# Kernel optimization log

Hardware: AMD Instinct MI355X
Metric: run time of the kernel (lower is better)

## Reference

```python
import jax, jax.numpy as jnp
import numpy as np

N_USERS = 50000
N_ITEMS = 75000
N_NODES = N_USERS + N_ITEMS
NNZ = 1250000
EMB = 64
N_LAYERS = 3
BATCH = 4096
EPS = 1e-12


def setup_inputs() -> dict:
    key = jax.random.key(0)
    ks = jax.random.split(key, 12)
    xavier = float(np.sqrt(6.0 / (EMB + EMB)))
    return {
        "user": jax.random.randint(ks[0], (BATCH,), 0, N_USERS, dtype=jnp.int64 if jax.config.jax_enable_x64 else jnp.int32),
        "pos_item": jax.random.randint(ks[1], (BATCH,), 0, N_ITEMS, dtype=jnp.int32),
        "neg_item": jax.random.randint(ks[2], (BATCH,), 0, N_ITEMS, dtype=jnp.int32),
        "row": jax.random.randint(ks[3], (NNZ,), 0, N_NODES, dtype=jnp.int32),
        "col": jax.random.randint(ks[4], (NNZ,), 0, N_NODES, dtype=jnp.int32),
        "vals": jax.random.uniform(ks[5], (NNZ,), dtype=jnp.float32),
        "emb": jax.random.normal(ks[6], (N_NODES, EMB), dtype=jnp.float32) * 0.1,
        "W1": jax.random.uniform(ks[7], (N_LAYERS, EMB, EMB), minval=-xavier, maxval=xavier, dtype=jnp.float32),
        "b1": jnp.zeros((N_LAYERS, EMB), dtype=jnp.float32),
        "W2": jax.random.uniform(ks[8], (N_LAYERS, EMB, EMB), minval=-xavier, maxval=xavier, dtype=jnp.float32),
        "b2": jnp.zeros((N_LAYERS, EMB), dtype=jnp.float32),
    }


def _l2_normalize(x):
    n = jnp.linalg.norm(x, axis=-1, keepdims=True)
    return x / jnp.maximum(n, EPS)


def reference(user, pos_item, neg_item, row, col, vals, emb, W1, b1, W2, b2):
    # eval mode: node_dropout / mess_dropout inactive (rates 0)
    node_feat = emb
    all_embeddings = [node_feat]
    for l in range(N_LAYERS):
        # sparse SpMM: agg[i] = sum_j A[i,j] * node_feat[j]
        msg = vals[:, None] * node_feat[col]            # [nnz, d]
        agg = jax.ops.segment_sum(msg, row, num_segments=N_NODES)  # [N, d]
        part_1 = jax.nn.leaky_relu(agg @ W1[l].T + b1[l], 0.2)
        part_2 = jax.nn.leaky_relu((agg * node_feat) @ W2[l].T + b2[l], 0.2)
        node_feat = part_1 + part_2
        all_embeddings.append(_l2_normalize(node_feat))
    embedding_weight = jnp.concatenate(all_embeddings, axis=-1)  # [N, 4*d]
    gcn_user = embedding_weight[:N_USERS]
    gcn_item = embedding_weight[N_USERS:]
    return (gcn_user[user], gcn_item[pos_item], gcn_item[neg_item])
```

## Files before the change

kernel.cpp:

```cpp
#include <hip/hip_runtime.h>
#include <hip/hip_fp16.h>

#define N_USERS 50000
#define N_ITEMS 75000
#define N_NODES 125000
#define N_PAD   125008
#define NNZ     1250000
#define EMB     64
#define N_LAYERS 3
#define BATCH   4096
#define CONCAT  256

#define BROWS   128
#define NB      ((N_NODES + BROWS - 1) / BROWS)
#define CHUNK   4096
#define NCHUNK  ((NNZ + CHUNK - 1) / CHUNK)
#define EPT     (CHUNK / 256)
#define BCAP    1600
#define FB_NODES 32
#define SCAP    8

#define F4      (N_NODES * EMB / 4)
#define G4      (3 * BATCH * EMB / 4)
#define SM      (3 * BATCH)
#define INIT_ITEMS (F4 + G4 + SM)
#define INIT_BLOCKS ((INIT_ITEMS + 255) / 256)

typedef _Float16 half8  __attribute__((ext_vector_type(8)));
typedef _Float16 half4  __attribute__((ext_vector_type(4)));
typedef float    floatx4 __attribute__((ext_vector_type(4)));

__device__ __forceinline__ bool user_is_i64(const void* uptr) {
    const int* u = (const int*)uptr;
    return (u[1] | u[3] | u[5] | u[7]) == 0;
}
__device__ __forceinline__ int load_user(const void* uptr, int b, bool is64) {
    return is64 ? (int)((const long long*)uptr)[b] : ((const int*)uptr)[b];
}
__device__ __forceinline__ int sample_node(const void* user, const int* pos,
                                           const int* neg, int which, int b,
                                           bool is64) {
    if (which == 0) return load_user(user, b, is64);
    return N_USERS + (which == 1 ? pos[b] : neg[b]);
}

__device__ __forceinline__ float unpack_val(unsigned w) {
    unsigned short us = (unsigned short)(w >> 17);
    _Float16 h = __builtin_bit_cast(_Float16, us);
    return (float)h;
}

__global__ __launch_bounds__(256) void part_init_kernel(
    const int* __restrict__ row, const int* __restrict__ col,
    const float* __restrict__ vals, const float* __restrict__ emb,
    const void* __restrict__ user, const int* __restrict__ pos,
    const int* __restrict__ neg,
    _Float16* __restrict__ f16, float* __restrict__ out,
    int* __restrict__ bcnt, int* __restrict__ scnt, int* __restrict__ smap,
    unsigned long long* __restrict__ sw8) {

    __shared__ int h[NB];
    __shared__ int base[NB];

    if (blockIdx.x < NCHUNK) {
        int t = threadIdx.x;
        int e0 = blockIdx.x * CHUNK;
        int e1 = e0 + CHUNK; if (e1 > NNZ) e1 = NNZ;
        for (int i = t; i < NB; i += 256) h[i] = 0;
        __syncthreads();

        unsigned long long rec[EPT];
        int bkt[EPT];
        int ps[EPT];
        int cnt = 0;
        for (int e = e0 + t; e < e1; e += 256) {
            int r = row[e];
            int b = r >> 7;
            _Float16 hv = (_Float16)vals[e];
            unsigned hb = (unsigned)__builtin_bit_cast(unsigned short, hv);
            rec[cnt] = ((unsigned long long)hb << 24)
                     | ((unsigned)(r & 127) << 17)
                     | (unsigned)col[e];
            bkt[cnt] = b;
            ps[cnt] = atomicAdd(&h[b], 1);
            ++cnt;
        }
        __syncthreads();
        for (int i = t; i < NB; i += 256) {
            int c = h[i];
            if (c) base[i] = atomicAdd(&bcnt[i], c);
        }
        __syncthreads();
        for (int k = 0; k < cnt; ++k) {
            int b = bkt[k];
            sw8[(size_t)b * BCAP + base[b] + ps[k]] = rec[k];
        }
    } else {
        int idx = (blockIdx.x - NCHUNK) * 256 + threadIdx.x;
        bool is64 = user_is_i64(user);
        if (idx < F4) {
            floatx4 v = *(const floatx4*)(emb + (size_t)idx * 4);
            half4 o;
            #pragma unroll
            for (int i = 0; i < 4; ++i) o[i] = (_Float16)v[i];
            *(half4*)(f16 + (size_t)idx * 4) = o;
        } else if (idx < F4 + G4) {
            int j = idx - F4;
            int which = j / (BATCH * 16);
            int rem   = j % (BATCH * 16);
            int bb = rem >> 4, c4 = rem & 15;
            int node = sample_node(user, pos, neg, which, bb, is64);
            floatx4 v = *(const floatx4*)(emb + (size_t)node * EMB + c4 * 4);
            *(floatx4*)(out + (size_t)(which * BATCH + bb) * CONCAT + c4 * 4) = v;
        } else if (idx < F4 + G4 + SM) {
            int g2 = idx - F4 - G4;
            int which = g2 / BATCH, bb = g2 % BATCH;
            int node = sample_node(user, pos, neg, which, bb, is64);
            int slot = atomicAdd(&scnt[node], 1);
            if (slot < SCAP) smap[node * SCAP + slot] = g2;
        }
    }
}

__global__ __launch_bounds__(256) void bucket_sort_kernel(
    const int* __restrict__ bcnt,
    const unsigned long long* __restrict__ sw8,
    unsigned* __restrict__ se, int* __restrict__ off, int* __restrict__ endv) {
    __shared__ unsigned long long ew[BCAP];
    __shared__ unsigned eo[BCAP];
    __shared__ int rh[BROWS], rb[BROWS], rc[BROWS];
    __shared__ int s[256];

    int b = blockIdx.x, t = threadIdx.x;
    int n = bcnt[b];
    int s0 = b * BCAP;
    if (t < BROWS) rh[t] = 0;
    __syncthreads();
    const unsigned long long* src = sw8 + (size_t)b * BCAP;
    for (int i = t; i < n; i += 256) {
        unsigned long long rec = src[i];
        ew[i] = rec;
        atomicAdd(&rh[(int)((rec >> 17) & 127)], 1);
    }
    __syncthreads();
    s[t] = (t < BROWS) ? rh[t] : 0;
    __syncthreads();
    for (int d = 1; d < 256; d <<= 1) {
        int x = (t >= d) ? s[t - d] : 0;
        __syncthreads();
        s[t] += x;
        __syncthreads();
    }
    if (t < BROWS) {
        int excl = s[t] - rh[t];
        rb[t] = excl;
        rc[t] = 0;
        int r = b * BROWS + t;
        if (r < N_NODES) {
            off[r]  = s0 + excl;
            endv[r] = s0 + s[t];
        }
    }
    __syncthreads();
    for (int i = t; i < n; i += 256) {
        unsigned long long rec = ew[i];
        int r = (int)((rec >> 17) & 127);
        int p = rb[r] + atomicAdd(&rc[r], 1);
        eo[p] = (unsigned)(((rec >> 24) << 17) | (rec & 0x1FFFFULL));
    }
    __syncthreads();
    for (int i = t; i < n; i += 256)
        se[(size_t)s0 + i] = eo[i];
}

__global__ __launch_bounds__(256) void layer_kernel(
    const int* __restrict__ off, const int* __restrict__ endv,
    const unsigned* __restrict__ se,
    const _Float16* __restrict__ fin, _Float16* __restrict__ fout,
    const float* __restrict__ W1, const float* __restrict__ b1,
    const float* __restrict__ W2, const float* __restrict__ b2,
    const int* __restrict__ scnt, const int* __restrict__ smap,
    float* __restrict__ out, int layer) {

    __shared__ _Float16 wlds[2][EMB][EMB];
    __shared__ _Float16 alds[FB_NODES][EMB];

    int tid = threadIdx.x;

    {
        const float* Wsrc0 = W1 + layer * EMB * EMB;
        const float* Wsrc1 = W2 + layer * EMB * EMB;
        #pragma unroll
        for (int m = 0; m < 2; ++m) {
            const float* Ws = m ? Wsrc1 : Wsrc0;
            for (int c = tid; c < 512; c += 256) {
                int n = c >> 3, c16 = c & 7;
                const float* p = Ws + n * EMB + c16 * 8;
                floatx4 wa = *(const floatx4*)p, wb = *(const floatx4*)(p + 4);
                half8 h;
                #pragma unroll
                for (int i = 0; i < 4; ++i) {
                    h[i] = (_Float16)wa[i]; h[4 + i] = (_Float16)wb[i];
                }
                *(half8*)(&wlds[m][n][(c16 ^ (n & 7)) * 8]) = h;
            }
        }
    }

    int wave = tid >> 6, lane = tid & 63;
    int g = lane >> 3;
    int k = lane & 7;
    int base = blockIdx.x * FB_NODES;
    int ln = wave * 8 + g;
    int node = base + ln;
    bool valid = node < N_NODES;

    int j   = valid ? off[node]  : 0;
    int end = valid ? endv[node] : 0;

    float acc[8] = {0.f, 0.f, 0.f, 0.f, 0.f, 0.f, 0.f, 0.f};
    const _Float16* fink = fin + k * 8;

    while (__any(j < end)) {
        unsigned ev[8];
        #pragma unroll
        for (int t = 0; t < 8; ++t)
            ev[t] = (j + t < end) ? se[j + t] : 0u;
        half8 h[8];
        #pragma unroll
        for (int t = 0; t < 8; ++t) {
            int c = (int)(ev[t] & 0x1FFFFu);
            h[t] = *(const half8*)(fink + (size_t)c * EMB);
        }
        #pragma unroll
        for (int t = 0; t < 8; ++t) {
            float val = unpack_val(ev[t]);
            #pragma unroll
            for (int i = 0; i < 8; ++i)
                acc[i] += (float)h[t][i] * val;
        }
        j += 8;
    }

    {
        half8 o;
        #pragma unroll
        for (int i = 0; i < 8; ++i) o[i] = (_Float16)acc[i];
        *(half8*)(&alds[ln][(k ^ (ln & 7)) * 8]) = o;
    }
    __syncthreads();

    if (wave < 2) {
        int lm = lane & 15, quad = lane >> 4;
        int ln0 = wave * 16 + lm;
        int nb = base + wave * 16;
        int nodeD = nb + lm;
        int sw = lm & 7;

        half8 a0 = *(const half8*)(&alds[ln0][(quad ^ sw) * 8]);
        half8 a1 = *(const half8*)(&alds[ln0][((quad + 4) ^ sw) * 8]);

        int nsafe = nodeD < N_NODES ? nodeD : 0;
        const half8* fp = (const half8*)(fin + (size_t)nsafe * EMB + quad * 8);
        half8 f0 = fp[0], f1 = fp[4];
        half8 g0 = a0 * f0, g1 = a1 * f1;

        float nfv[4][4];
        float sq[4] = {0.f, 0.f, 0.f, 0.f};

        #pragma unroll
        for (int t = 0; t < 4; ++t) {
            int n = t * 16 + lm;
            float bias1 = b1[layer * EMB + n];
            float bias2 = b2[layer * EMB + n];
            half8 w10 = *(const half8*)(&wlds[0][n][(quad ^ sw) * 8]);
            half8 w11 = *(const half8*)(&wlds[0][n][((quad + 4) ^ sw) * 8]);
            half8 w20 = *(const half8*)(&wlds[1][n][(quad ^ sw) * 8]);
            half8 w21 = *(const half8*)(&wlds[1][n][((quad + 4) ^ sw) * 8]);
            floatx4 d1 = {0.f, 0.f, 0.f, 0.f}, d2 = {0.f, 0.f, 0.f, 0.f};
            d1 = __builtin_amdgcn_mfma_f32_16x16x32_f16(a0, w10, d1, 0, 0, 0);
            d1 = __builtin_amdgcn_mfma_f32_16x16x32_f16(a1, w11, d1, 0, 0, 0);
            d2 = __builtin_amdgcn_mfma_f32_16x16x32_f16(g0, w20, d2, 0, 0, 0);
            d2 = __builtin_amdgcn_mfma_f32_16x16x32_f16(g1, w21, d2, 0, 0, 0);
            int dim = t * 16 + lm;
            #pragma unroll
            for (int r = 0; r < 4; ++r) {
                int nodeO = nb + quad * 4 + r;
                float p1v = d1[r] + bias1;
                p1v = p1v > 0.f ? p1v : 0.2f * p1v;
                float p2v = d2[r] + bias2;
                p2v = p2v > 0.f ? p2v : 0.2f * p2v;
                float nf = p1v + p2v;
                nfv[t][r] = nf;
                sq[r] += nf * nf;
                if (layer != N_LAYERS - 1 && nodeO < N_NODES)
                    fout[(size_t)nodeO * EMB + dim] = (_Float16)nf;
            }
        }

        #pragma unroll
        for (int r = 0; r < 4; ++r) {
            float v = sq[r];
            #pragma unroll
            for (int m = 1; m < 16; m <<= 1) v += __shfl_xor(v, m, 64);
            sq[r] = fmaxf(sqrtf(v), 1e-12f);
        }

        #pragma unroll
        for (int r = 0; r < 4; ++r) {
            int nodeO = nb + quad * 4 + r;
            if (nodeO >= N_NODES) continue;
            int c = scnt[nodeO]; c = c < SCAP ? c : SCAP;
            float inv = 1.0f / sq[r];
            for (int i2 = 0; i2 < c; ++i2) {
                int smp = smap[nodeO * SCAP + i2];
                float* po = out + (size_t)smp * CONCAT + (layer + 1) * EMB;
                #pragma unroll
                for (int t = 0; t < 4; ++t)
                    po[t * 16 + lm] = nfv[t][r] * inv;
            }
        }
    }
}

extern "C" void kernel_launch(void* const* d_in, const int* in_sizes, int n_in,
                              void* d_out, int out_size, void* d_ws, size_t ws_size,
                              hipStream_t stream) {
    const void* user = d_in[0];
    const int* pos  = (const int*)d_in[1];
    const int* neg  = (const int*)d_in[2];
    const int* row  = (const int*)d_in[3];
    const int* col  = (const int*)d_in[4];
    const float* vals = (const float*)d_in[5];
    const float* emb  = (const float*)d_in[6];
    const float* W1   = (const float*)d_in[7];
    const float* b1   = (const float*)d_in[8];
    const float* W2   = (const float*)d_in[9];
    const float* b2   = (const float*)d_in[10];

    _Float16* f16a   = (_Float16*)d_ws;
    _Float16* f16b   = f16a + (size_t)N_PAD * EMB;
    int*      off    = (int*)(f16b + (size_t)N_PAD * EMB);
    int*      endv   = off + (N_NODES + 8);
    int*      bcnt   = endv + (N_NODES + 8);
    int*      scnt   = bcnt + 984;
    int*      smap   = scnt + N_NODES;
    unsigned long long* sw8 = (unsigned long long*)(smap + N_NODES * SCAP);
    unsigned* se     = (unsigned*)(sw8 + (size_t)NB * BCAP);

    float* out = (float*)d_out;

    hipMemsetAsync(bcnt, 0, (size_t)(984 + N_NODES) * sizeof(int), stream);

    part_init_kernel<<<NCHUNK + INIT_BLOCKS, 256, 0, stream>>>(
        row, col, vals, emb, user, pos, neg, f16a, out, bcnt, scnt, smap, sw8);

    bucket_sort_kernel<<<NB, 256, 0, stream>>>(bcnt, sw8, se, off, endv);

    const _Float16* fin = f16a;
    _Float16* fout = f16b;
    for (int l = 0; l < N_LAYERS; ++l) {
        layer_kernel<<<(N_NODES + FB_NODES - 1) / FB_NODES, 256, 0, stream>>>(
            off, endv, se, fin, fout, W1, b1, W2, b2, scnt, smap, out, l);
        const _Float16* tmp = fout; fout = (_Float16*)fin; fin = (const _Float16*)tmp;
    }
}
```

Baseline: 245.9 us.

## Reorder nodes by degree class and process 64 nodes per block

After: 268.0 us. 1.09x slower.

```diff
diff --git a/kernel.cpp b/kernel.cpp
--- a/kernel.cpp
+++ b/kernel.cpp
@@ -17,8 +17,10 @@
 #define NCHUNK  ((NNZ + CHUNK - 1) / CHUNK)
 #define EPT     (CHUNK / 256)
 #define BCAP    1600
-#define FB_NODES 32
+#define FB_NODES 64
+#define NT64    ((N_NODES + FB_NODES - 1) / FB_NODES)
 #define SCAP    8
+#define NCLS    8
 
 #define F4      (N_NODES * EMB / 4)
 #define G4      (3 * BATCH * EMB / 4)
@@ -125,16 +127,19 @@
 __global__ __launch_bounds__(256) void bucket_sort_kernel(
     const int* __restrict__ bcnt,
     const unsigned long long* __restrict__ sw8,
-    unsigned* __restrict__ se, int* __restrict__ off, int* __restrict__ endv) {
+    unsigned* __restrict__ se, int* __restrict__ off, int* __restrict__ endv,
+    int* __restrict__ classcnt) {
     __shared__ unsigned long long ew[BCAP];
     __shared__ unsigned eo[BCAP];
     __shared__ int rh[BROWS], rb[BROWS], rc[BROWS];
     __shared__ int s[256];
+    __shared__ int ch[NCLS];
 
     int b = blockIdx.x, t = threadIdx.x;
     int n = bcnt[b];
     int s0 = b * BCAP;
     if (t < BROWS) rh[t] = 0;
+    if (t >= BROWS && t < BROWS + NCLS) ch[t - BROWS] = 0;
     __syncthreads();
     const unsigned long long* src = sw8 + (size_t)b * BCAP;
     for (int i = t; i < n; i += 256) {
@@ -159,9 +164,12 @@
         if (r < N_NODES) {
             off[r]  = s0 + excl;
             endv[r] = s0 + s[t];
-        }
-    }
-    __syncthreads();
+            int c = (rh[t] + 7) >> 3; if (c > NCLS - 1) c = NCLS - 1;
+            atomicAdd(&ch[c], 1);
+        }
+    }
+    __syncthreads();
+    if (t < NCLS && ch[t]) atomicAdd(&classcnt[t], ch[t]);
     for (int i = t; i < n; i += 256) {
         unsigned long long rec = ew[i];
         int r = (int)((rec >> 17) & 127);
@@ -173,9 +181,35 @@
         se[(size_t)s0 + i] = eo[i];
 }
 
+__global__ __launch_bounds__(256) void perm_kernel(
+    const int* __restrict__ off, const int* __restrict__ endv,
+    const int* __restrict__ classcnt, int* __restrict__ classpos,
+    int* __restrict__ perm) {
+    __shared__ int lh[NCLS], lbase[NCLS];
+    int t = threadIdx.x;
+    int node = blockIdx.x * 256 + t;
+    if (t < NCLS) lh[t] = 0;
+    __syncthreads();
+    int c = -1, lpos = 0;
+    if (node < N_NODES) {
+        int deg = endv[node] - off[node];
+        c = (deg + 7) >> 3; if (c > NCLS - 1) c = NCLS - 1;
+        lpos = atomicAdd(&lh[c], 1);
+    }
+    __syncthreads();
+    if (t < NCLS) {
+        int sbase = 0;
+        #pragma unroll
+        for (int i = 0; i < NCLS; ++i) if (i < t) sbase += classcnt[i];
+        lbase[t] = sbase + (lh[t] ? atomicAdd(&classpos[t], lh[t]) : 0);
+    }
+    __syncthreads();
+    if (node < N_NODES) perm[lbase[c] + lpos] = node;
+}
+
 __global__ __launch_bounds__(256) void layer_kernel(
     const int* __restrict__ off, const int* __restrict__ endv,
-    const unsigned* __restrict__ se,
+    const unsigned* __restrict__ se, const int* __restrict__ perm,
     const _Float16* __restrict__ fin, _Float16* __restrict__ fout,
     const float* __restrict__ W1, const float* __restrict__ b1,
     const float* __restrict__ W2, const float* __restrict__ b2,
@@ -211,38 +245,36 @@
     int g = lane >> 3;
     int k = lane & 7;
     int base = blockIdx.x * FB_NODES;
-    int ln = wave * 8 + g;
-    int node = base + ln;
-    bool valid = node < N_NODES;
-
-    int j   = valid ? off[node]  : 0;
-    int end = valid ? endv[node] : 0;
-
-    float acc[8] = {0.f, 0.f, 0.f, 0.f, 0.f, 0.f, 0.f, 0.f};
     const _Float16* fink = fin + k * 8;
 
-    while (__any(j < end)) {
-        unsigned ev[8];
-        #pragma unroll
-        for (int t = 0; t < 8; ++t)
-            ev[t] = (j + t < end) ? se[j + t] : 0u;
-        half8 h[8];
-        #pragma unroll
-        for (int t = 0; t < 8; ++t) {
-            int c = (int)(ev[t] & 0x1FFFFu);
-            h[t] = *(const half8*)(fink + (size_t)c * EMB);
-        }
-        #pragma unroll
-        for (int t = 0; t < 8; ++t) {
-            float val = unpack_val(ev[t]);
-            #pragma unroll
-            for (int i = 0; i < 8; ++i)
-                acc[i] += (float)h[t][i] * val;
-        }
-        j += 8;
-    }
-
-    {
+    for (int p = 0; p < 2; ++p) {
+        int ln = p * 32 + wave * 8 + g;
+        int idx = base + ln;
+        int node = (idx < N_NODES) ? perm[idx] : -1;
+        int j = 0, end = 0;
+        if (node >= 0) { j = off[node]; end = endv[node]; }
+
+        float acc[8] = {0.f, 0.f, 0.f, 0.f, 0.f, 0.f, 0.f, 0.f};
+        while (__any(j < end)) {
+            unsigned ev[8];
+            #pragma unroll
+            for (int t = 0; t < 8; ++t)
+                ev[t] = (j + t < end) ? se[j + t] : 0u;
+            half8 h[8];
+            #pragma unroll
+            for (int t = 0; t < 8; ++t) {
+                int c = (int)(ev[t] & 0x1FFFFu);
+                h[t] = *(const half8*)(fink + (size_t)c * EMB);
+            }
+            #pragma unroll
+            for (int t = 0; t < 8; ++t) {
+                float val = unpack_val(ev[t]);
+                #pragma unroll
+                for (int i = 0; i < 8; ++i)
+                    acc[i] += (float)h[t][i] * val;
+            }
+            j += 8;
+        }
         half8 o;
         #pragma unroll
         for (int i = 0; i < 8; ++i) o[i] = (_Float16)acc[i];
@@ -250,17 +282,17 @@
     }
     __syncthreads();
 
-    if (wave < 2) {
+    {
         int lm = lane & 15, quad = lane >> 4;
         int ln0 = wave * 16 + lm;
-        int nb = base + wave * 16;
-        int nodeD = nb + lm;
+        int idxD = base + ln0;
+        int nodeD = (idxD < N_NODES) ? perm[idxD] : -1;
         int sw = lm & 7;
 
         half8 a0 = *(const half8*)(&alds[ln0][(quad ^ sw) * 8]);
         half8 a1 = *(const half8*)(&alds[ln0][((quad + 4) ^ sw) * 8]);
 
-        int nsafe = nodeD < N_NODES ? nodeD : 0;
+        int nsafe = nodeD >= 0 ? nodeD : 0;
         const half8* fp = (const half8*)(fin + (size_t)nsafe * EMB + quad * 8);
         half8 f0 = fp[0], f1 = fp[4];
         half8 g0 = a0 * f0, g1 = a1 * f1;
@@ -282,10 +314,8 @@
             d1 = __builtin_amdgcn_mfma_f32_16x16x32_f16(a1, w11, d1, 0, 0, 0);
             d2 = __builtin_amdgcn_mfma_f32_16x16x32_f16(g0, w20, d2, 0, 0, 0);
             d2 = __builtin_amdgcn_mfma_f32_16x16x32_f16(g1, w21, d2, 0, 0, 0);
-            int dim = t * 16 + lm;
             #pragma unroll
             for (int r = 0; r < 4; ++r) {
-                int nodeO = nb + quad * 4 + r;
                 float p1v = d1[r] + bias1;
                 p1v = p1v > 0.f ? p1v : 0.2f * p1v;
                 float p2v = d2[r] + bias2;
@@ -293,8 +323,22 @@
                 float nf = p1v + p2v;
                 nfv[t][r] = nf;
                 sq[r] += nf * nf;
-                if (layer != N_LAYERS - 1 && nodeO < N_NODES)
-                    fout[(size_t)nodeO * EMB + dim] = (_Float16)nf;
+            }
+        }
+
+        int nodeO[4];
+        #pragma unroll
+        for (int r = 0; r < 4; ++r)
+            nodeO[r] = __shfl(nodeD, quad * 4 + r, 64);
+
+        if (layer != N_LAYERS - 1) {
+            #pragma unroll
+            for (int t = 0; t < 4; ++t) {
+                int dim = t * 16 + lm;
+                #pragma unroll
+                for (int r = 0; r < 4; ++r)
+                    if (nodeO[r] >= 0)
+                        fout[(size_t)nodeO[r] * EMB + dim] = (_Float16)nfv[t][r];
             }
         }
 
@@ -308,12 +352,11 @@
 
         #pragma unroll
         for (int r = 0; r < 4; ++r) {
-            int nodeO = nb + quad * 4 + r;
-            if (nodeO >= N_NODES) continue;
-            int c = scnt[nodeO]; c = c < SCAP ? c : SCAP;
+            if (nodeO[r] < 0) continue;
+            int c = scnt[nodeO[r]]; c = c < SCAP ? c : SCAP;
             float inv = 1.0f / sq[r];
             for (int i2 = 0; i2 < c; ++i2) {
-                int smp = smap[nodeO * SCAP + i2];
+                int smp = smap[nodeO[r] * SCAP + i2];
                 float* po = out + (size_t)smp * CONCAT + (layer + 1) * EMB;
                 #pragma unroll
                 for (int t = 0; t < 4; ++t)
@@ -342,26 +385,32 @@
     _Float16* f16b   = f16a + (size_t)N_PAD * EMB;
     int*      off    = (int*)(f16b + (size_t)N_PAD * EMB);
     int*      endv   = off + (N_NODES + 8);
-    int*      bcnt   = endv + (N_NODES + 8);
+    int*      perm   = endv + (N_NODES + 8);
+    int*      bcnt   = perm + N_NODES;
     int*      scnt   = bcnt + 984;
-    int*      smap   = scnt + N_NODES;
+    int*      classcnt = scnt + N_NODES;
+    int*      classpos = classcnt + NCLS;
+    int*      smap   = classpos + NCLS;
     unsigned long long* sw8 = (unsigned long long*)(smap + N_NODES * SCAP);
     unsigned* se     = (unsigned*)(sw8 + (size_t)NB * BCAP);
 
     float* out = (float*)d_out;
 
-    hipMemsetAsync(bcnt, 0, (size_t)(984 + N_NODES) * sizeof(int), stream);
+    hipMemsetAsync(bcnt, 0, (size_t)(984 + N_NODES + 2 * NCLS) * sizeof(int), stream);
 
     part_init_kernel<<<NCHUNK + INIT_BLOCKS, 256, 0, stream>>>(
         row, col, vals, emb, user, pos, neg, f16a, out, bcnt, scnt, smap, sw8);
 
-    bucket_sort_kernel<<<NB, 256, 0, stream>>>(bcnt, sw8, se, off, endv);
+    bucket_sort_kernel<<<NB, 256, 0, stream>>>(bcnt, sw8, se, off, endv, classcnt);
+
+    perm_kernel<<<(N_NODES + 255) / 256, 256, 0, stream>>>(
+        off, endv, classcnt, classpos, perm);
 
     const _Float16* fin = f16a;
     _Float16* fout = f16b;
     for (int l = 0; l < N_LAYERS; ++l) {
-        layer_kernel<<<(N_NODES + FB_NODES - 1) / FB_NODES, 256, 0, stream>>>(
-            off, endv, se, fin, fout, W1, b1, W2, b2, scnt, smap, out, l);
+        layer_kernel<<<NT64, 256, 0, stream>>>(
+            off, endv, se, perm, fin, fout, W1, b1, W2, b2, scnt, smap, out, l);
         const _Float16* tmp = fout; fout = (_Float16*)fin; fin = (const _Float16*)tmp;
     }
 }
```

## Grow layer blocks to 128 nodes with 512 threads and prefetch edge records

Applied to the files above, without the earlier changes.

New measurement: 294.6 us. +19.8%, slower.

```diff
diff --git a/kernel.cpp b/kernel.cpp
--- a/kernel.cpp
+++ b/kernel.cpp
@@ -17,7 +17,8 @@
 #define NCHUNK  ((NNZ + CHUNK - 1) / CHUNK)
 #define EPT     (CHUNK / 256)
 #define BCAP    1600
-#define FB_NODES 32
+#define FB_NODES 128
+#define NBLK    ((N_NODES + FB_NODES - 1) / FB_NODES)
 #define SCAP    8
 
 #define F4      (N_NODES * EMB / 4)
@@ -173,7 +174,7 @@
         se[(size_t)s0 + i] = eo[i];
 }
 
-__global__ __launch_bounds__(256) void layer_kernel(
+__global__ __launch_bounds__(512, 8) void layer_kernel(
     const int* __restrict__ off, const int* __restrict__ endv,
     const unsigned* __restrict__ se,
     const _Float16* __restrict__ fin, _Float16* __restrict__ fout,
@@ -193,7 +194,8 @@
         #pragma unroll
         for (int m = 0; m < 2; ++m) {
             const float* Ws = m ? Wsrc1 : Wsrc0;
-            for (int c = tid; c < 512; c += 256) {
+            int c = tid & 511;
+            if (c < 512) {
                 int n = c >> 3, c16 = c & 7;
                 const float* p = Ws + n * EMB + c16 * 8;
                 floatx4 wa = *(const floatx4*)p, wb = *(const floatx4*)(p + 4);
@@ -211,38 +213,43 @@
     int g = lane >> 3;
     int k = lane & 7;
     int base = blockIdx.x * FB_NODES;
-    int ln = wave * 8 + g;
-    int node = base + ln;
-    bool valid = node < N_NODES;
-
-    int j   = valid ? off[node]  : 0;
-    int end = valid ? endv[node] : 0;
-
-    float acc[8] = {0.f, 0.f, 0.f, 0.f, 0.f, 0.f, 0.f, 0.f};
     const _Float16* fink = fin + k * 8;
 
-    while (__any(j < end)) {
+    for (int p = 0; p < 2; ++p) {
+        int ln = p * 64 + wave * 8 + g;
+        int node = base + ln;
+        bool valid = node < N_NODES;
+        int j   = valid ? off[node]  : 0;
+        int end = valid ? endv[node] : 0;
+
+        float acc[8] = {0.f, 0.f, 0.f, 0.f, 0.f, 0.f, 0.f, 0.f};
         unsigned ev[8];
         #pragma unroll
         for (int t = 0; t < 8; ++t)
             ev[t] = (j + t < end) ? se[j + t] : 0u;
-        half8 h[8];
-        #pragma unroll
-        for (int t = 0; t < 8; ++t) {
-            int c = (int)(ev[t] & 0x1FFFFu);
-            h[t] = *(const half8*)(fink + (size_t)c * EMB);
-        }
-        #pragma unroll
-        for (int t = 0; t < 8; ++t) {
-            float val = unpack_val(ev[t]);
-            #pragma unroll
-            for (int i = 0; i < 8; ++i)
-                acc[i] += (float)h[t][i] * val;
-        }
-        j += 8;
-    }
-
-    {
+
+        while (__any(j < end)) {
+            int jn = j + 8;
+            half8 h[8];
+            #pragma unroll
+            for (int t = 0; t < 8; ++t) {
+                int c = (int)(ev[t] & 0x1FFFFu);
+                h[t] = *(const half8*)(fink + (size_t)c * EMB);
+            }
+            unsigned evn[8];
+            #pragma unroll
+            for (int t = 0; t < 8; ++t)
+                evn[t] = (jn + t < end) ? se[jn + t] : 0u;
+            #pragma unroll
+            for (int t = 0; t < 8; ++t) {
+                float val = unpack_val(ev[t]);
+                #pragma unroll
+                for (int i = 0; i < 8; ++i)
+                    acc[i] += (float)h[t][i] * val;
+                ev[t] = evn[t];
+            }
+            j = jn;
+        }
         half8 o;
         #pragma unroll
         for (int i = 0; i < 8; ++i) o[i] = (_Float16)acc[i];
@@ -250,7 +257,7 @@
     }
     __syncthreads();
 
-    if (wave < 2) {
+    {
         int lm = lane & 15, quad = lane >> 4;
         int ln0 = wave * 16 + lm;
         int nb = base + wave * 16;
@@ -282,10 +289,8 @@
             d1 = __builtin_amdgcn_mfma_f32_16x16x32_f16(a1, w11, d1, 0, 0, 0);
             d2 = __builtin_amdgcn_mfma_f32_16x16x32_f16(g0, w20, d2, 0, 0, 0);
             d2 = __builtin_amdgcn_mfma_f32_16x16x32_f16(g1, w21, d2, 0, 0, 0);
-            int dim = t * 16 + lm;
             #pragma unroll
             for (int r = 0; r < 4; ++r) {
-                int nodeO = nb + quad * 4 + r;
                 float p1v = d1[r] + bias1;
                 p1v = p1v > 0.f ? p1v : 0.2f * p1v;
                 float p2v = d2[r] + bias2;
@@ -293,8 +298,19 @@
                 float nf = p1v + p2v;
                 nfv[t][r] = nf;
                 sq[r] += nf * nf;
-                if (layer != N_LAYERS - 1 && nodeO < N_NODES)
-                    fout[(size_t)nodeO * EMB + dim] = (_Float16)nf;
+            }
+        }
+
+        if (layer != N_LAYERS - 1) {
+            #pragma unroll
+            for (int t = 0; t < 4; ++t) {
+                int dim = t * 16 + lm;
+                #pragma unroll
+                for (int r = 0; r < 4; ++r) {
+                    int nodeO = nb + quad * 4 + r;
+                    if (nodeO < N_NODES)
+                        fout[(size_t)nodeO * EMB + dim] = (_Float16)nfv[t][r];
+                }
             }
         }
 
@@ -360,7 +376,7 @@
     const _Float16* fin = f16a;
     _Float16* fout = f16b;
     for (int l = 0; l < N_LAYERS; ++l) {
-        layer_kernel<<<(N_NODES + FB_NODES - 1) / FB_NODES, 256, 0, stream>>>(
+        layer_kernel<<<NBLK, 512, 0, stream>>>(
             off, endv, se, fin, fout, W1, b1, W2, b2, scnt, smap, out, l);
         const _Float16* tmp = fout; fout = (_Float16*)fin; fin = (const _Float16*)tmp;
     }
```
